# Optimization experiments

Hardware: AMD Instinct MI355X
Metric: run time of the kernel (lower is better)

## Reference

```python
import jax, jax.numpy as jnp
import numpy as np

B, N = 128, 196
HDIM, VDIM, ATT = 512, 2048, 512


def setup_inputs() -> dict:
    key = jax.random.key(0)
    ks = jax.random.split(key, 8)
    s_w = 1.0 / np.sqrt(HDIM)
    s_u = 1.0 / np.sqrt(VDIM)
    s_v = 1.0 / np.sqrt(ATT)
    return {
        "h": jax.random.normal(ks[0], (B, HDIM), dtype=jnp.float32),
        "V": jax.random.normal(ks[1], (B, N, VDIM), dtype=jnp.float32),
        "Ww": jax.random.uniform(ks[2], (HDIM, ATT), jnp.float32, -s_w, s_w),
        "Wb": jax.random.uniform(ks[3], (ATT,), jnp.float32, -s_w, s_w),
        "Uw": jax.random.uniform(ks[4], (VDIM, ATT), jnp.float32, -s_u, s_u),
        "Ub": jax.random.uniform(ks[5], (ATT,), jnp.float32, -s_u, s_u),
        "vw": jax.random.uniform(ks[6], (ATT, 1), jnp.float32, -s_v, s_v),
        "vb": jax.random.uniform(ks[7], (1,), jnp.float32, -s_v, s_v),
    }


def reference(h, V, Ww, Wb, Uw, Ub, vw, vb):
    # W(h): [B, A]; U(V): [B, N, A]
    wh = h @ Ww + Wb
    uv = jnp.einsum("bnv,va->bna", V, Uw) + Ub
    # e: [B, N, 1] scores via v(tanh(...))
    e = jnp.tanh(wh[:, None, :] + uv) @ vw + vb
    a = jax.nn.softmax(e, axis=1)          # softmax over N locations
    ctx = jnp.sum(a * V, axis=1)            # [B, vdim]
    return ctx, a.squeeze(-1)
```

## Files before the change

### kernel.cpp

```cpp
#include <hip/hip_runtime.h>
#include <hip/hip_bf16.h>

#define B_    128
#define N_    196
#define HDIM  512
#define VDIM  2048
#define ATT   512
#define M_TOT (B_ * N_)

#define BKK 64
#define NT  (VDIM / BKK)
#define BM1 128
#define BN1 128
#define BM2 256
#define BN2 256
#define N8     ((B_ * N_ * VDIM) / 8)
#define NCONVB 12544

typedef float  f32x4  __attribute__((ext_vector_type(4)));
typedef __bf16 bf16x8 __attribute__((ext_vector_type(8)));
typedef __bf16 bf16x4 __attribute__((ext_vector_type(4)));

__device__ __forceinline__ void gload_lds16(const void* g, void* l) {
    __builtin_amdgcn_global_load_lds(
        (const __attribute__((address_space(1))) void*)g,
        (__attribute__((address_space(3))) void*)l, 16, 0, 0);
}

__device__ __forceinline__ float fast_tanh(float x) {
    float ax = fabsf(x);
    float e  = __expf(-2.f * ax);
    float t  = (1.f - e) / (1.f + e);
    return copysignf(t, x);
}

__global__ void k_convprep(const float* __restrict__ V, __bf16* __restrict__ Vb,
                           const float* __restrict__ Uw, __bf16* __restrict__ UwT,
                           const float* __restrict__ h, const float* __restrict__ Ww,
                           const float* __restrict__ Wb, const float* __restrict__ Ub,
                           float* __restrict__ whp) {
    int t = threadIdx.x;
    if (blockIdx.x < 128) {
        __shared__ float hs[HDIM];
        int b = blockIdx.x;
        hs[t]       = h[(size_t)b * HDIM + t];
        hs[t + 256] = h[(size_t)b * HDIM + t + 256];
        __syncthreads();
        float a0[8] = {0,0,0,0,0,0,0,0}, a1[8] = {0,0,0,0,0,0,0,0};
        for (int k0 = 0; k0 < HDIM; k0 += 8) {
#pragma unroll
            for (int u = 0; u < 8; ++u) {
                float hv = hs[k0 + u];
                a0[u] += hv * Ww[(size_t)(k0 + u) * ATT + t];
                a1[u] += hv * Ww[(size_t)(k0 + u) * ATT + t + 256];
            }
        }
        float s0 = ((a0[0] + a0[1]) + (a0[2] + a0[3])) + ((a0[4] + a0[5]) + (a0[6] + a0[7]));
        float s1 = ((a1[0] + a1[1]) + (a1[2] + a1[3])) + ((a1[4] + a1[5]) + (a1[6] + a1[7]));
        whp[(size_t)b * ATT + t]       = s0 + Wb[t] + Ub[t];
        whp[(size_t)b * ATT + t + 256] = s1 + Wb[t + 256] + Ub[t + 256];
    } else if (blockIdx.x < 384) {
        __shared__ __bf16 st[64][65];
        int bb = blockIdx.x - 128;
        int k0 = (bb & 31) * 64;
        int c0 = (bb >> 5) * 64;
#pragma unroll
        for (int i = 0; i < 16; ++i) {
            int lin = i * 256 + t;
            int kk = lin >> 6, cc = lin & 63;
            st[kk][cc] = (__bf16)Uw[(size_t)(k0 + kk) * ATT + c0 + cc];
        }
        __syncthreads();
#pragma unroll
        for (int i = 0; i < 16; ++i) {
            int lin = i * 256 + t;
            int cc = lin >> 6, kk = lin & 63;
            UwT[(size_t)(c0 + cc) * VDIM + k0 + kk] = st[kk][cc];
        }
    } else {
        size_t base = (size_t)(blockIdx.x - 384) * 256 + t;
        const float4* Vp = reinterpret_cast<const float4*>(V);
        float4 xs[2], ys[2];
#pragma unroll
        for (int u = 0; u < 2; ++u) {
            size_t i = base + (size_t)u * ((size_t)NCONVB * 256);
            xs[u] = Vp[2 * i];
            ys[u] = Vp[2 * i + 1];
        }
#pragma unroll
        for (int u = 0; u < 2; ++u) {
            size_t i = base + (size_t)u * ((size_t)NCONVB * 256);
            float4 x = xs[u], y = ys[u];
            bf16x8 w;
            w[0] = (__bf16)x.x; w[1] = (__bf16)x.y; w[2] = (__bf16)x.z; w[3] = (__bf16)x.w;
            w[4] = (__bf16)y.x; w[5] = (__bf16)y.y; w[6] = (__bf16)y.z; w[7] = (__bf16)y.w;
            reinterpret_cast<bf16x8*>(Vb)[i] = w;
        }
    }
}

__global__ __launch_bounds__(512, 2) void k_scores256(
    const __bf16* __restrict__ Vb, const __bf16* __restrict__ UwT,
    const float* __restrict__ whp, const float* __restrict__ vw,
    float* __restrict__ e_part)
{
    __shared__ __align__(16) __bf16 As[2][BM2][BKK];
    __shared__ __align__(16) __bf16 Bs[2][BN2][BKK];
    __shared__ float red[4][BM2];

    int bid = blockIdx.x;
    int xcd = bid & 7, ix = bid >> 3;
    int lid = (xcd < 4 ? xcd * 25 : 100 + (xcd - 4) * 24) + ix;
    int mtile = lid >> 1;
    int cc    = lid & 1;
    int m0 = mtile * BM2;
    int c0 = cc * BN2;

    int t    = threadIdx.x;
    int lane = t & 63;
    int wave = t >> 6;
    int wr = wave >> 2;
    int wc = wave & 3;

    f32x4 acc[8][4];
#pragma unroll
    for (int i = 0; i < 8; ++i)
#pragma unroll
        for (int j = 0; j < 4; ++j) acc[i][j] = (f32x4){0.f, 0.f, 0.f, 0.f};

    int lr  = lane >> 3;
    int csw = ((lane & 7) ^ lr) * 8;
    const __bf16* AgS = Vb  + (size_t)(m0 + wave * 32 + lr) * VDIM + csw;
    const __bf16* BgS = UwT + (size_t)(c0 + wave * 32 + lr) * VDIM + csw;
    __bf16* Al0 = &As[0][wave * 32 + lr][(lane & 7) * 8];
    __bf16* Bl0 = &Bs[0][wave * 32 + lr][(lane & 7) * 8];

#define STAGE2(buf, kt)                                                         \
    do {                                                                        \
        _Pragma("unroll")                                                       \
        for (int i = 0; i < 4; ++i) {                                           \
            gload_lds16(AgS + (kt) * BKK + (size_t)i * 8 * VDIM,                \
                        Al0 + (buf) * (BM2 * BKK) + i * 8 * BKK);               \
            gload_lds16(BgS + (kt) * BKK + (size_t)i * 8 * VDIM,                \
                        Bl0 + (buf) * (BN2 * BKK) + i * 8 * BKK);               \
        }                                                                       \
    } while (0)

    int lcol = lane & 15;
    int lg4  = lane >> 4;
    int arow0 = wr * 128;
    int bcol0 = wc * 64;

    STAGE2(0, 0);
    __builtin_amdgcn_sched_barrier(0);
    STAGE2(1, 1);

    for (int kt = 0; kt < NT; ++kt) {
        int buf = kt & 1;
        if (kt < NT - 1) {
            asm volatile("s_waitcnt vmcnt(8)\n\ts_barrier" ::: "memory");
        } else {
            asm volatile("s_waitcnt vmcnt(0)\n\ts_barrier" ::: "memory");
        }
        __builtin_amdgcn_sched_barrier(0);

#pragma unroll
        for (int ks = 0; ks < 2; ++ks) {
            bf16x8 bfr[4], af[8];
#pragma unroll
            for (int j = 0; j < 4; ++j) {
                int row = bcol0 + j * 16 + lcol;
                int ch  = ((ks * 4 + lg4) ^ (row & 7)) * 8;
                bfr[j] = *reinterpret_cast<const bf16x8*>(&Bs[buf][row][ch]);
            }
#pragma unroll
            for (int i = 0; i < 8; ++i) {
                int row = arow0 + i * 16 + lcol;
                int ch  = ((ks * 4 + lg4) ^ (row & 7)) * 8;
                af[i] = *reinterpret_cast<const bf16x8*>(&As[buf][row][ch]);
            }
            __builtin_amdgcn_s_setprio(1);
#pragma unroll
            for (int i = 0; i < 8; ++i)
#pragma unroll
                for (int j = 0; j < 4; ++j)
                    acc[i][j] = __builtin_amdgcn_mfma_f32_16x16x32_bf16(af[i], bfr[j], acc[i][j], 0, 0, 0);
            __builtin_amdgcn_s_setprio(0);
        }

        __builtin_amdgcn_sched_barrier(0);
        asm volatile("s_barrier" ::: "memory");
        if (kt + 2 < NT) STAGE2(buf, kt + 2);
    }
#undef STAGE2

    int lrow4 = lg4 * 4;
#pragma unroll
    for (int i = 0; i < 8; ++i) {
        float rs[4] = {0.f, 0.f, 0.f, 0.f};
#pragma unroll
        for (int j = 0; j < 4; ++j) {
            int col = c0 + wc * 64 + j * 16 + lcol;
            float vwv = vw[col];
#pragma unroll
            for (int r = 0; r < 4; ++r) {
                int m = m0 + wr * 128 + i * 16 + lrow4 + r;
                int b = m / N_;
                float x = acc[i][j][r] + whp[(size_t)b * ATT + col];
                rs[r] += fast_tanh(x) * vwv;
            }
        }
#pragma unroll
        for (int r = 0; r < 4; ++r) {
            float v = rs[r];
            v += __shfl_xor(v, 1);
            v += __shfl_xor(v, 2);
            v += __shfl_xor(v, 4);
            v += __shfl_xor(v, 8);
            if (lcol == 0)
                red[wc][wr * 128 + i * 16 + lrow4 + r] = v;
        }
    }
    __syncthreads();
    if (t < BM2)
        e_part[(size_t)cc * M_TOT + m0 + t] =
            red[0][t] + red[1][t] + red[2][t] + red[3][t];
}

__global__ __launch_bounds__(256, 2) void k_scores_small(
    const float* __restrict__ Vf, const __bf16* __restrict__ UwT,
    const float* __restrict__ whp, const float* __restrict__ vw,
    float* __restrict__ e_part)
{
    __shared__ __align__(16) __bf16 As[2][BM1][BKK];
    __shared__ __align__(16) __bf16 Bs[2][BN1][BKK];
    __shared__ float red[2][BM1];

    int bid = blockIdx.x;
    int lid = (bid & 7) * (784 / 8) + (bid >> 3);
    int mtile = lid >> 2;
    int cc    = lid & 3;
    int m0 = mtile * BM1;
    int c0 = cc * BN1;
    int t    = threadIdx.x;
    int lane = t & 63;
    int wave = t >> 6;
    int wr = wave >> 1;
    int wc = wave & 1;

    f32x4 acc[4][4];
#pragma unroll
    for (int i = 0; i < 4; ++i)
#pragma unroll
        for (int j = 0; j < 4; ++j) acc[i][j] = (f32x4){0.f, 0.f, 0.f, 0.f};

    int lr  = lane >> 3;
    int csw = ((lane & 7) ^ lr) * 8;
    const __bf16* BgS = UwT + (size_t)(c0 + wave * 32 + lr) * VDIM + csw;
    __bf16* Bl0 = &Bs[0][wave * 32 + lr][(lane & 7) * 8];

    int ra = t >> 1;
    int ka = (t & 1) * 32;
    const float* Af = Vf + (size_t)(m0 + ra) * VDIM + ka;

#define STAGE1(buf, kt)                                                         \
    do {                                                                        \
        _Pragma("unroll")                                                       \
        for (int i = 0; i < 4; ++i)                                             \
            gload_lds16(BgS + (kt) * BKK + (size_t)i * 8 * VDIM,                \
                        Bl0 + (buf) * (BN1 * BKK) + i * 8 * BKK);               \
        const float4* src = reinterpret_cast<const float4*>(Af + (kt) * BKK);   \
        _Pragma("unroll")                                                       \
        for (int i = 0; i < 4; ++i) {                                           \
            float4 x = src[2 * i];                                              \
            float4 y = src[2 * i + 1];                                          \
            bf16x8 w;                                                           \
            w[0] = (__bf16)x.x; w[1] = (__bf16)x.y;                             \
            w[2] = (__bf16)x.z; w[3] = (__bf16)x.w;                             \
            w[4] = (__bf16)y.x; w[5] = (__bf16)y.y;                             \
            w[6] = (__bf16)y.z; w[7] = (__bf16)y.w;                             \
            int ch = (((t & 1) * 4 + i) ^ (ra & 7)) * 8;                        \
            *reinterpret_cast<bf16x8*>(&As[buf][ra][ch]) = w;                   \
        }                                                                       \
    } while (0)

    int lcol = lane & 15;
    int lg4  = lane >> 4;
    int arow0 = wr * 64;
    int bcol0 = wc * 64;

    STAGE1(0, 0);
    __syncthreads();

    for (int kt = 0; kt < NT; ++kt) {
        int buf = kt & 1;
        if (kt + 1 < NT) STAGE1(buf ^ 1, kt + 1);
#pragma unroll
        for (int ks = 0; ks < 2; ++ks) {
            bf16x8 af[4], bfr[4];
#pragma unroll
            for (int i = 0; i < 4; ++i) {
                int row = arow0 + i * 16 + lcol;
                int ch  = ((ks * 4 + lg4) ^ (row & 7)) * 8;
                af[i] = *reinterpret_cast<const bf16x8*>(&As[buf][row][ch]);
            }
#pragma unroll
            for (int j = 0; j < 4; ++j) {
                int row = bcol0 + j * 16 + lcol;
                int ch  = ((ks * 4 + lg4) ^ (row & 7)) * 8;
                bfr[j] = *reinterpret_cast<const bf16x8*>(&Bs[buf][row][ch]);
            }
#pragma unroll
            for (int i = 0; i < 4; ++i)
#pragma unroll
                for (int j = 0; j < 4; ++j)
                    acc[i][j] = __builtin_amdgcn_mfma_f32_16x16x32_bf16(af[i], bfr[j], acc[i][j], 0, 0, 0);
        }
        __syncthreads();
    }
#undef STAGE1

    int lrow4 = lg4 * 4;
#pragma unroll
    for (int i = 0; i < 4; ++i) {
        float rs[4] = {0.f, 0.f, 0.f, 0.f};
#pragma unroll
        for (int j = 0; j < 4; ++j) {
            int col = c0 + wc * 64 + j * 16 + lcol;
            float vwv = vw[col];
#pragma unroll
            for (int r = 0; r < 4; ++r) {
                int m = m0 + wr * 64 + i * 16 + lrow4 + r;
                int b = m / N_;
                float x = acc[i][j][r] + whp[(size_t)b * ATT + col];
                rs[r] += fast_tanh(x) * vwv;
            }
        }
#pragma unroll
        for (int r = 0; r < 4; ++r) {
            float v = rs[r];
            v += __shfl_xor(v, 1);
            v += __shfl_xor(v, 2);
            v += __shfl_xor(v, 4);
            v += __shfl_xor(v, 8);
            if (lcol == 0)
                red[wc][wr * 64 + i * 16 + lrow4 + r] = v;
        }
    }
    __syncthreads();
    if (t < BM1)
        e_part[(size_t)cc * M_TOT + m0 + t] = red[0][t] + red[1][t];
}

__global__ void k_ctx_sm(const __bf16* __restrict__ Vb, const float* __restrict__ e_part,
                         const float* __restrict__ vb, float* __restrict__ a_out,
                         float* __restrict__ ctx, int npart) {
    int b  = blockIdx.x;
    int ch = blockIdx.y;
    int t  = threadIdx.x;
    __shared__ float sm[256];
    __shared__ float as_[N_];

    float ev = 0.f;
    float e  = -1e30f;
    if (t < N_) {
        int m = b * N_ + t;
        ev = vb[0];
        for (int p = 0; p < npart; ++p) ev += e_part[(size_t)p * M_TOT + m];
        e = ev;
    }
    sm[t] = e;
    __syncthreads();
    for (int s = 128; s > 0; s >>= 1) {
        if (t < s) sm[t] = fmaxf(sm[t], sm[t + s]);
        __syncthreads();
    }
    float mx = sm[0];
    __syncthreads();
    float ex = (t < N_) ? __expf(ev - mx) : 0.f;
    sm[t] = ex;
    __syncthreads();
    for (int s = 128; s > 0; s >>= 1) {
        if (t < s) sm[t] += sm[t + s];
        __syncthreads();
    }
    float inv = 1.f / sm[0];
    if (t < N_) {
        as_[t] = ex * inv;
        if (ch == 0) a_out[(size_t)b * N_ + t] = ex * inv;
    }
    __syncthreads();

    int col = ch * 1024 + t * 4;
    const __bf16* Vp = Vb + (size_t)b * N_ * VDIM + col;
    float av[4] = {0.f, 0.f, 0.f, 0.f};
    for (int n = 0; n < N_; ++n) {
        bf16x4 v = *reinterpret_cast<const bf16x4*>(Vp + (size_t)n * VDIM);
        float an = as_[n];
#pragma unroll
        for (int j = 0; j < 4; ++j) av[j] += an * (float)v[j];
    }
    f32x4 o = {av[0], av[1], av[2], av[3]};
    *reinterpret_cast<f32x4*>(ctx + (size_t)b * VDIM + col) = o;
}

__global__ void k_softmax(const float* __restrict__ e_part, const float* __restrict__ vb,
                          float* __restrict__ a_out) {
    int b = blockIdx.x;
    int t = threadIdx.x;
    __shared__ float sm[256];
    float ev = 0.f;
    float e  = -1e30f;
    if (t < N_) {
        int m = b * N_ + t;
        ev = e_part[m] + e_part[M_TOT + m] + e_part[2 * M_TOT + m] + e_part[3 * M_TOT + m] + vb[0];
        e = ev;
    }
    sm[t] = e;
    __syncthreads();
    for (int s = 128; s > 0; s >>= 1) {
        if (t < s) sm[t] = fmaxf(sm[t], sm[t + s]);
        __syncthreads();
    }
    float mx = sm[0];
    __syncthreads();
    float ex = (t < N_) ? __expf(ev - mx) : 0.f;
    sm[t] = ex;
    __syncthreads();
    for (int s = 128; s > 0; s >>= 1) {
        if (t < s) sm[t] += sm[t + s];
        __syncthreads();
    }
    float inv = 1.f / sm[0];
    if (t < N_) a_out[(size_t)b * N_ + t] = ex * inv;
}

__global__ void k_ctx_f32(const float* __restrict__ V, const float* __restrict__ a,
                          float* __restrict__ ctx) {
    int b  = blockIdx.x;
    int ch = blockIdx.y;
    int t  = threadIdx.x;
    __shared__ float as_[N_];
    for (int i = t; i < N_; i += 128) as_[i] = a[(size_t)b * N_ + i];
    __syncthreads();
    int col = ch * 512 + t * 4;
    const f32x4* Vp = reinterpret_cast<const f32x4*>(V + (size_t)b * N_ * VDIM + col);
    f32x4 accv = {0.f, 0.f, 0.f, 0.f};
    for (int n = 0; n < N_; ++n)
        accv += as_[n] * Vp[(size_t)n * (VDIM / 4)];
    *reinterpret_cast<f32x4*>(ctx + (size_t)b * VDIM + col) = accv;
}

extern "C" void kernel_launch(void* const* d_in, const int* in_sizes, int n_in,
                              void* d_out, int out_size, void* d_ws, size_t ws_size,
                              hipStream_t stream) {
    const float* h  = (const float*)d_in[0];
    const float* V  = (const float*)d_in[1];
    const float* Ww = (const float*)d_in[2];
    const float* Wb = (const float*)d_in[3];
    const float* Uw = (const float*)d_in[4];
    const float* Ub = (const float*)d_in[5];
    const float* vw = (const float*)d_in[6];
    const float* vb = (const float*)d_in[7];

    float* out     = (float*)d_out;
    float* ctx_out = out;
    float* a_out   = out + (size_t)B_ * VDIM;

    const size_t vb_bytes = (size_t)B_ * N_ * VDIM * sizeof(__bf16);
    const size_t tail     = 2u * 1024 * 1024 + 256 * 1024 + (size_t)4 * M_TOT * 4 + 4096;
    bool preconv = ws_size >= vb_bytes + tail;

    char*   ws   = (char*)d_ws;
    __bf16* Vb   = (__bf16*)ws;
    char*   rest = ws + (preconv ? vb_bytes : 0);
    __bf16* UwT   = (__bf16*)rest;
    float*  whp   = (float*)(rest + 2u * 1024 * 1024);
    float*  e_prt = (float*)(rest + 2u * 1024 * 1024 + 256 * 1024);

    int grid_cp = preconv ? (384 + NCONVB) : 384;
    k_convprep<<<dim3(grid_cp), 256, 0, stream>>>(
        V, Vb, Uw, UwT, h, Ww, Wb, Ub, whp);
    if (preconv) {
        k_scores256<<<dim3(196), 512, 0, stream>>>(Vb, UwT, whp, vw, e_prt);
        k_ctx_sm<<<dim3(B_, 2), 256, 0, stream>>>(Vb, e_prt, vb, a_out, ctx_out, 2);
    } else {
        k_scores_small<<<dim3(784), 256, 0, stream>>>(V, UwT, whp, vw, e_prt);
        k_softmax<<<dim3(B_), 256, 0, stream>>>(e_prt, vb, a_out);
        k_ctx_f32<<<dim3(B_, 4), 128, 0, stream>>>(V, a_out, ctx_out);
    }
}
```

Before: 143.4 us.

## Use 4-stage K=32 LDS ring in score GEMM, dropping second barrier

Replaces the double-buffered K=64 LDS pipeline in the scores GEMM with a 4-deep ring of K=32 slices. The next stage is prefetched three slices ahead and issued right after the wait barrier, so the trailing per-iteration s_barrier is removed. The XOR swizzle is adapted to 4 chunks per row. LDS usage stays the same, but there are twice as many loop iterations and waitcnt/barrier points, and a 4-way swizzle may leave more bank conflicts on the fragment reads.

```diff
diff --git a/kernel.cpp b/kernel.cpp
--- a/kernel.cpp
+++ b/kernel.cpp
@@ -10,6 +10,8 @@
 
 #define BKK 64
 #define NT  (VDIM / BKK)
+#define BKK2 32
+#define NT2 (VDIM / BKK2)
 #define BM1 128
 #define BN1 128
 #define BM2 256
@@ -104,8 +106,8 @@
     const float* __restrict__ whp, const float* __restrict__ vw,
     float* __restrict__ e_part)
 {
-    __shared__ __align__(16) __bf16 As[2][BM2][BKK];
-    __shared__ __align__(16) __bf16 Bs[2][BN2][BKK];
+    __shared__ __align__(16) __bf16 As[4][BM2][BKK2];
+    __shared__ __align__(16) __bf16 Bs[4][BN2][BKK2];
     __shared__ float red[4][BM2];
 
     int bid = blockIdx.x;
@@ -128,21 +130,21 @@
 #pragma unroll
         for (int j = 0; j < 4; ++j) acc[i][j] = (f32x4){0.f, 0.f, 0.f, 0.f};
 
-    int lr  = lane >> 3;
-    int csw = ((lane & 7) ^ lr) * 8;
-    const __bf16* AgS = Vb  + (size_t)(m0 + wave * 32 + lr) * VDIM + csw;
-    const __bf16* BgS = UwT + (size_t)(c0 + wave * 32 + lr) * VDIM + csw;
-    __bf16* Al0 = &As[0][wave * 32 + lr][(lane & 7) * 8];
-    __bf16* Bl0 = &Bs[0][wave * 32 + lr][(lane & 7) * 8];
+    int lrA = lane >> 2;
+    int chA = ((lane & 3) ^ (lrA & 3)) * 8;
+    const __bf16* AgS = Vb  + (size_t)(m0 + wave * 32 + lrA) * VDIM + chA;
+    const __bf16* BgS = UwT + (size_t)(c0 + wave * 32 + lrA) * VDIM + chA;
+    __bf16* Al0 = &As[0][wave * 32 + lrA][(lane & 3) * 8];
+    __bf16* Bl0 = &Bs[0][wave * 32 + lrA][(lane & 3) * 8];
 
 #define STAGE2(buf, kt)                                                         \
     do {                                                                        \
         _Pragma("unroll")                                                       \
-        for (int i = 0; i < 4; ++i) {                                           \
-            gload_lds16(AgS + (kt) * BKK + (size_t)i * 8 * VDIM,                \
-                        Al0 + (buf) * (BM2 * BKK) + i * 8 * BKK);               \
-            gload_lds16(BgS + (kt) * BKK + (size_t)i * 8 * VDIM,                \
-                        Bl0 + (buf) * (BN2 * BKK) + i * 8 * BKK);               \
+        for (int i = 0; i < 2; ++i) {                                           \
+            gload_lds16(AgS + (kt) * BKK2 + (size_t)i * 16 * VDIM,              \
+                        Al0 + (buf) * (BM2 * BKK2) + i * 16 * BKK2);            \
+            gload_lds16(BgS + (kt) * BKK2 + (size_t)i * 16 * VDIM,              \
+                        Bl0 + (buf) * (BN2 * BKK2) + i * 16 * BKK2);            \
         }                                                                       \
     } while (0)
 
@@ -150,47 +152,42 @@
     int lg4  = lane >> 4;
     int arow0 = wr * 128;
     int bcol0 = wc * 64;
+    int chR   = (lg4 ^ (lcol & 3)) * 8;
 
     STAGE2(0, 0);
     __builtin_amdgcn_sched_barrier(0);
     STAGE2(1, 1);
-
-    for (int kt = 0; kt < NT; ++kt) {
-        int buf = kt & 1;
-        if (kt < NT - 1) {
+    __builtin_amdgcn_sched_barrier(0);
+    STAGE2(2, 2);
+
+    for (int kt = 0; kt < NT2; ++kt) {
+        int buf = kt & 3;
+        if (kt < NT2 - 2) {
             asm volatile("s_waitcnt vmcnt(8)\n\ts_barrier" ::: "memory");
+        } else if (kt == NT2 - 2) {
+            asm volatile("s_waitcnt vmcnt(4)\n\ts_barrier" ::: "memory");
         } else {
             asm volatile("s_waitcnt vmcnt(0)\n\ts_barrier" ::: "memory");
         }
         __builtin_amdgcn_sched_barrier(0);
 
-#pragma unroll
-        for (int ks = 0; ks < 2; ++ks) {
-            bf16x8 bfr[4], af[8];
-#pragma unroll
-            for (int j = 0; j < 4; ++j) {
-                int row = bcol0 + j * 16 + lcol;
-                int ch  = ((ks * 4 + lg4) ^ (row & 7)) * 8;
-                bfr[j] = *reinterpret_cast<const bf16x8*>(&Bs[buf][row][ch]);
-            }
-#pragma unroll
-            for (int i = 0; i < 8; ++i) {
-                int row = arow0 + i * 16 + lcol;
-                int ch  = ((ks * 4 + lg4) ^ (row & 7)) * 8;
-                af[i] = *reinterpret_cast<const bf16x8*>(&As[buf][row][ch]);
-            }
-            __builtin_amdgcn_s_setprio(1);
-#pragma unroll
-            for (int i = 0; i < 8; ++i)
-#pragma unroll
-                for (int j = 0; j < 4; ++j)
-                    acc[i][j] = __builtin_amdgcn_mfma_f32_16x16x32_bf16(af[i], bfr[j], acc[i][j], 0, 0, 0);
-            __builtin_amdgcn_s_setprio(0);
-        }
-
+        if (kt + 3 < NT2) STAGE2((kt + 3) & 3, kt + 3);
+
+        bf16x8 bfr[4], af[8];
+#pragma unroll
+        for (int j = 0; j < 4; ++j)
+            bfr[j] = *reinterpret_cast<const bf16x8*>(&Bs[buf][bcol0 + j * 16 + lcol][chR]);
+#pragma unroll
+        for (int i = 0; i < 8; ++i)
+            af[i] = *reinterpret_cast<const bf16x8*>(&As[buf][arow0 + i * 16 + lcol][chR]);
+        __builtin_amdgcn_s_setprio(1);
+#pragma unroll
+        for (int i = 0; i < 8; ++i)
+#pragma unroll
+            for (int j = 0; j < 4; ++j)
+                acc[i][j] = __builtin_amdgcn_mfma_f32_16x16x32_bf16(af[i], bfr[j], acc[i][j], 0, 0, 0);
+        __builtin_amdgcn_s_setprio(0);
         __builtin_amdgcn_sched_barrier(0);
-        asm volatile("s_barrier" ::: "memory");
-        if (kt + 2 < NT) STAGE2(buf, kt + 2);
     }
 #undef STAGE2
 
```

Result: slower. 163.9 us (+14.3%).
